# Optimization experiments

Hardware: AMD Instinct MI355X
Metric: run time of the kernel (lower is better)

The kernel has to match this reference:

```python
import jax, jax.numpy as jnp
import numpy as np

HIDDEN = 2048
NUM_HEADS = 16
HEAD_DIM = 128
WINDOW_SIZE = 512
NUM_GLOBAL = 16
SCALING = HEAD_DIM ** -0.5


def setup_inputs() -> dict:
    key = jax.random.key(0)
    ks = jax.random.split(key, 5)
    std = HIDDEN ** -0.5
    hidden_states = jax.random.normal(ks[0], (1, 4096, HIDDEN), dtype=jnp.float32)
    # Linear weights stored as (in, out) so y = x @ W
    Wq = jax.random.normal(ks[1], (HIDDEN, NUM_HEADS * HEAD_DIM), dtype=jnp.float32) * std
    Wk = jax.random.normal(ks[2], (HIDDEN, NUM_HEADS * HEAD_DIM), dtype=jnp.float32) * std
    Wv = jax.random.normal(ks[3], (HIDDEN, NUM_HEADS * HEAD_DIM), dtype=jnp.float32) * std
    Wo = jax.random.normal(ks[4], (NUM_HEADS * HEAD_DIM, HIDDEN), dtype=jnp.float32) * std
    return {"hidden_states": hidden_states, "Wq": Wq, "Wk": Wk, "Wv": Wv, "Wo": Wo}


def _sliding_mask(q_len: int, kv_len: int) -> jnp.ndarray:
    q_pos = jnp.arange(q_len)[:, None]
    kv_pos = jnp.arange(kv_len)[None, :]
    half_window = WINDOW_SIZE // 2
    local = jnp.abs(q_pos - kv_pos) < half_window
    glob = (q_pos < NUM_GLOBAL) | (kv_pos < NUM_GLOBAL)
    mask = local | glob
    return jnp.where(mask, 0.0, -jnp.inf).astype(jnp.float32)


def reference(hidden_states, Wq, Wk, Wv, Wo):
    bsz, q_len, _ = hidden_states.shape
    q = (hidden_states @ Wq).reshape(bsz, q_len, NUM_HEADS, HEAD_DIM).transpose(0, 2, 1, 3)
    k = (hidden_states @ Wk).reshape(bsz, q_len, NUM_HEADS, HEAD_DIM).transpose(0, 2, 1, 3)
    v = (hidden_states @ Wv).reshape(bsz, q_len, NUM_HEADS, HEAD_DIM).transpose(0, 2, 1, 3)
    mask = _sliding_mask(q_len, q_len)[None, None]  # [1,1,S,S]
    scores = jnp.einsum("bhqd,bhkd->bhqk", q, k) * SCALING + mask
    attn = jax.nn.softmax(scores.astype(jnp.float32), axis=-1).astype(q.dtype)
    out = jnp.einsum("bhqk,bhkd->bhqd", attn, v)
    out = out.transpose(0, 2, 1, 3).reshape(bsz, q_len, NUM_HEADS * HEAD_DIM)
    return out @ Wo
```

## Files before the change

kernel.cpp:

```cpp
#include <hip/hip_runtime.h>
#include <stdint.h>

#define SEQ    4096
#define HID    2048
#define NQKV   6144
#define QKW    4096
#define NH     16
#define HD     128
#define SCALE  0.08838834764831845f
#define GQC    32

typedef unsigned short u16;
typedef __attribute__((ext_vector_type(8))) short bf16x8;
typedef __attribute__((ext_vector_type(4))) float f32x4;

__device__ __forceinline__ u16 f2bf(float f) {
  union { float f; unsigned u; } v; v.f = f;
  unsigned r = v.u + 0x7FFFu + ((v.u >> 16) & 1u);
  return (u16)(r >> 16);
}

__device__ __forceinline__ float bf2f(u16 b) {
  union { unsigned u; float f; } c; c.u = ((unsigned)b) << 16; return c.f;
}

__device__ __forceinline__ void async16(const u16* g, u16* l) {
  __builtin_amdgcn_global_load_lds(
      (const __attribute__((address_space(1))) unsigned int*)g,
      (__attribute__((address_space(3))) unsigned int*)l, 16, 0, 0);
}

__global__ __launch_bounds__(256) void prep(const float* __restrict__ X,
                                            const float* __restrict__ W0,
                                            const float* __restrict__ W1,
                                            const float* __restrict__ W2,
                                            const float* __restrict__ W3,
                                            u16* __restrict__ Xbf,
                                            u16* __restrict__ Wcat,
                                            u16* __restrict__ Wot,
                                            unsigned* __restrict__ cnt) {
  const int bx = blockIdx.x;
  const int t = threadIdx.x;
  if (bx == 0 && t < NH) cnt[t] = 0u;
  if (bx < 8192) {
    int i = bx * 256 + t;
    float4 v = ((const float4*)X)[i];
    ushort4 o;
    o.x = f2bf(v.x); o.y = f2bf(v.y); o.z = f2bf(v.z); o.w = f2bf(v.w);
    ((ushort4*)Xbf)[i] = o;
    return;
  }
  __shared__ __align__(16) u16 Ts[64 * 68];
  const int b = bx - 8192;
  const int z = b >> 10;
  const int k0 = ((b >> 5) & 31) * 64;
  const int n0 = (b & 31) * 64;
  const float* W = (z == 0) ? W0 : (z == 1) ? W1 : (z == 2) ? W2 : W3;
  u16* Wt = (z < 3) ? (Wcat + (size_t)z * 2048 * 2048) : Wot;
#pragma unroll
  for (int p = 0; p < 4; ++p) {
    int f = (t + p * 256) * 4;
    int r = f >> 6, c = f & 63;
    float4 v = *(const float4*)&W[(size_t)(k0 + r) * 2048 + n0 + c];
    ushort4 o; o.x = f2bf(v.x); o.y = f2bf(v.y); o.z = f2bf(v.z); o.w = f2bf(v.w);
    *(ushort4*)&Ts[r * 68 + c] = o;
  }
  __syncthreads();
#pragma unroll
  for (int p = 0; p < 4; ++p) {
    int g = (t + p * 256) * 4;
    int r = g >> 6, c = g & 63;
    ushort4 o;
    o.x = Ts[(c + 0) * 68 + r];
    o.y = Ts[(c + 1) * 68 + r];
    o.z = Ts[(c + 2) * 68 + r];
    o.w = Ts[(c + 3) * 68 + r];
    *(ushort4*)&Wt[(size_t)(n0 + r) * 2048 + k0 + c] = o;
  }
}

template <typename OutT, bool WVT>
__global__ __launch_bounds__(256) void gemm_bt(const u16* __restrict__ A,
                                               const u16* __restrict__ B,
                                               OutT* __restrict__ C,
                                               u16* __restrict__ VTout,
                                               int K, int ldc) {
  __shared__ __align__(16) u16 As0[128 * 32];
  __shared__ __align__(16) u16 As1[128 * 32];
  __shared__ __align__(16) u16 Bs0[128 * 32];
  __shared__ __align__(16) u16 Bs1[128 * 32];
  const int m0 = blockIdx.y * 128;
  const int n0 = blockIdx.x * 128;
  const int tid = threadIdx.x;
  const int wid = tid >> 6;
  const int lane = tid & 63;
  const int wm = wid & 1, wn = wid >> 1;
  const int l15 = lane & 15, g4 = lane >> 4;

  const int srow = wid * 32 + (lane >> 2);
  const int scol = (lane & 3) * 8;

  f32x4 acc[4][4] = {};

  const u16* pa0 = &A[(size_t)(m0 + srow) * K + scol];
  const u16* pa1 = &A[(size_t)(m0 + srow + 16) * K + scol];
  const u16* pb0 = &B[(size_t)(n0 + srow) * K + scol];
  const u16* pb1 = &B[(size_t)(n0 + srow + 16) * K + scol];
  const int lo0 = (wid * 32) * 32, lo1 = (wid * 32 + 16) * 32;

  for (int kt = 0; kt < K; kt += 64) {
    __syncthreads();
    async16(pa0 + kt, &As0[lo0]);
    async16(pa1 + kt, &As0[lo1]);
    async16(pb0 + kt, &Bs0[lo0]);
    async16(pb1 + kt, &Bs0[lo1]);
    async16(pa0 + kt + 32, &As1[lo0]);
    async16(pa1 + kt + 32, &As1[lo1]);
    async16(pb0 + kt + 32, &Bs1[lo0]);
    async16(pb1 + kt + 32, &Bs1[lo1]);
    __syncthreads();
    {
      bf16x8 af[4], bfr[4];
#pragma unroll
      for (int i = 0; i < 4; ++i)
        af[i] = *(const bf16x8*)&As0[(wm * 64 + i * 16 + l15) * 32 + g4 * 8];
#pragma unroll
      for (int i = 0; i < 4; ++i)
        bfr[i] = *(const bf16x8*)&Bs0[(wn * 64 + i * 16 + l15) * 32 + g4 * 8];
#pragma unroll
      for (int mi = 0; mi < 4; ++mi)
#pragma unroll
        for (int ni = 0; ni < 4; ++ni)
          acc[mi][ni] = __builtin_amdgcn_mfma_f32_16x16x32_bf16(af[mi], bfr[ni], acc[mi][ni], 0, 0, 0);
    }
    {
      bf16x8 af[4], bfr[4];
#pragma unroll
      for (int i = 0; i < 4; ++i)
        af[i] = *(const bf16x8*)&As1[(wm * 64 + i * 16 + l15) * 32 + g4 * 8];
#pragma unroll
      for (int i = 0; i < 4; ++i)
        bfr[i] = *(const bf16x8*)&Bs1[(wn * 64 + i * 16 + l15) * 32 + g4 * 8];
#pragma unroll
      for (int mi = 0; mi < 4; ++mi)
#pragma unroll
        for (int ni = 0; ni < 4; ++ni)
          acc[mi][ni] = __builtin_amdgcn_mfma_f32_16x16x32_bf16(af[mi], bfr[ni], acc[mi][ni], 0, 0, 0);
    }
  }

  if (WVT && n0 >= QKW) {
#pragma unroll
    for (int mi = 0; mi < 4; ++mi)
#pragma unroll
      for (int ni = 0; ni < 4; ++ni) {
        const int nv = n0 - QKW + wn * 64 + ni * 16 + l15;
        const int hh = nv >> 7, dd = nv & 127;
        u16* base = &VTout[((size_t)hh * HD + dd) * SEQ];
        const int mb = m0 + wm * 64 + mi * 16 + g4 * 4;
        u16 pk[4];
#pragma unroll
        for (int r = 0; r < 4; ++r) pk[r] = f2bf(acc[mi][ni][r]);
        *(uint2*)&base[mb] = *(uint2*)pk;
      }
  } else {
#pragma unroll
    for (int mi = 0; mi < 4; ++mi)
#pragma unroll
      for (int ni = 0; ni < 4; ++ni) {
        const int n = n0 + wn * 64 + ni * 16 + l15;
#pragma unroll
        for (int r = 0; r < 4; ++r) {
          const int m = m0 + wm * 64 + mi * 16 + g4 * 4 + r;
          float v = acc[mi][ni][r];
          if constexpr (sizeof(OutT) == 2) {
            C[(size_t)m * ldc + n] = (OutT)f2bf(v);
          } else {
            C[(size_t)m * ldc + n] = v;
          }
        }
      }
  }
}

__device__ __forceinline__ void mfma16q(f32x4 (&q)[4][2],
                                        const bf16x8 (&a)[4][2],
                                        const bf16x8 (&b)[2][2]) {
#pragma unroll
  for (int fm = 0; fm < 4; ++fm)
#pragma unroll
    for (int fn = 0; fn < 2; ++fn) {
      q[fm][fn] = __builtin_amdgcn_mfma_f32_16x16x32_bf16(a[fm][0], b[fn][0], q[fm][fn], 0, 0, 0);
      q[fm][fn] = __builtin_amdgcn_mfma_f32_16x16x32_bf16(a[fm][1], b[fn][1], q[fm][fn], 0, 0, 0);
    }
}

#define GPRE() do { asm volatile("" ::: "memory"); __builtin_amdgcn_s_barrier(); \
  asm volatile("s_waitcnt lgkmcnt(0)" ::: "memory"); __builtin_amdgcn_sched_barrier(0); \
  __builtin_amdgcn_s_setprio(1); } while (0)
#define GPOST() do { __builtin_amdgcn_s_setprio(0); asm volatile("" ::: "memory"); \
  __builtin_amdgcn_s_barrier(); } while (0)
#define GPOSTVM() do { __builtin_amdgcn_s_setprio(0); \
  asm volatile("s_waitcnt vmcnt(4)" ::: "memory"); asm volatile("" ::: "memory"); \
  __builtin_amdgcn_s_barrier(); } while (0)

template <typename OutT, bool WVT>
__global__ __launch_bounds__(512, 2) void gemm256(const u16* __restrict__ A,
                                                  const u16* __restrict__ B,
                                                  OutT* __restrict__ C,
                                                  u16* __restrict__ VTout,
                                                  int K, int ldc) {
  __shared__ __align__(16) u16 As[2][2][128 * 64];
  __shared__ __align__(16) u16 Bs[2][2][128 * 64];
  const int m0 = blockIdx.y * 256;
  const int n0 = blockIdx.x * 256;
  const int tid = threadIdx.x;
  const int lane = tid & 63;
  const int wid = tid >> 6;
  const int wm = wid >> 2, wn = wid & 3;
  const int l15 = lane & 15, g4 = lane >> 4;

  const int r0 = tid >> 3;
  const int csw = ((tid & 7) ^ (r0 & 7)) * 8;
  const u16* Ag = A + (size_t)(m0 + r0) * K + csw;
  const u16* Bg = B + (size_t)(n0 + r0) * K + csw;

  const int aoff0 = (wm * 64 + l15) * 64;
  const int boff0 = (wn * 32 + l15) * 64;
  const int c0 = ((g4 ^ (l15 & 7)) << 3);
  const int c1 = (((4 + g4) ^ (l15 & 7)) << 3);

  auto stage = [&](const u16* src, int half, int tile, u16* dst) {
    const u16* s = src + (size_t)half * 128 * K + (size_t)tile * 64;
    u16* d = dst + wid * 512;
    async16(s, d);
    async16(s + (size_t)64 * K, d + 4096);
  };
  auto rdA = [&](const u16* h, bf16x8 (&a)[4][2]) {
#pragma unroll
    for (int fm = 0; fm < 4; ++fm) {
      a[fm][0] = *(const bf16x8*)&h[aoff0 + fm * 1024 + c0];
      a[fm][1] = *(const bf16x8*)&h[aoff0 + fm * 1024 + c1];
    }
  };
  auto rdB = [&](const u16* h, bf16x8 (&b)[2][2]) {
#pragma unroll
    for (int fn = 0; fn < 2; ++fn) {
      b[fn][0] = *(const bf16x8*)&h[boff0 + fn * 1024 + c0];
      b[fn][1] = *(const bf16x8*)&h[boff0 + fn * 1024 + c1];
    }
  };

  f32x4 acc[2][2][4][2] = {};

  stage(Ag, 0, 0, &As[0][0][0]);
  stage(Bg, 0, 0, &Bs[0][0][0]);
  stage(Ag, 1, 0, &As[0][1][0]);
  stage(Bg, 1, 0, &Bs[0][1][0]);
  stage(Ag, 0, 1, &As[1][0][0]);
  stage(Bg, 0, 1, &Bs[1][0][0]);
  asm volatile("s_waitcnt vmcnt(4)" ::: "memory");
  asm volatile("" ::: "memory");
  __builtin_amdgcn_s_barrier();

  const int NT = K >> 6;
  for (int it = 0; it < (NT >> 1); ++it) {
    const int tA = 2 * it + 1;
    const int tB = (2 * it + 2) & (NT - 1);
    const int tC = (2 * it + 3) & (NT - 1);
    {
      bf16x8 a0[4][2], a1[4][2], b0[2][2], b1[2][2];
      rdA(&As[0][0][0], a0); rdB(&Bs[0][0][0], b0);
      stage(Ag, 1, tA, &As[1][1][0]);
      asm volatile("s_waitcnt lgkmcnt(8)" ::: "memory");
      GPRE(); mfma16q(acc[0][0], a0, b0); GPOST();
      rdA(&As[0][1][0], a1);
      stage(Bg, 1, tA, &Bs[1][1][0]);
      GPRE(); mfma16q(acc[1][0], a1, b0); GPOST();
      rdB(&Bs[0][1][0], b1);
      stage(Ag, 0, tB, &As[0][0][0]);
      GPRE(); mfma16q(acc[0][1], a0, b1); GPOST();
      stage(Bg, 0, tB, &Bs[0][0][0]);
      GPRE(); mfma16q(acc[1][1], a1, b1); GPOSTVM();
    }
    {
      bf16x8 a0[4][2], a1[4][2], b0[2][2], b1[2][2];
      rdA(&As[1][0][0], a0); rdB(&Bs[1][0][0], b0);
      stage(Ag, 1, tB, &As[0][1][0]);
      asm volatile("s_waitcnt lgkmcnt(8)" ::: "memory");
      GPRE(); mfma16q(acc[0][0], a0, b0); GPOST();
      rdA(&As[1][1][0], a1);
      stage(Bg, 1, tB, &Bs[0][1][0]);
      GPRE(); mfma16q(acc[1][0], a1, b0); GPOST();
      rdB(&Bs[1][1][0], b1);
      stage(Ag, 0, tC, &As[1][0][0]);
      GPRE(); mfma16q(acc[0][1], a0, b1); GPOST();
      stage(Bg, 0, tC, &Bs[1][0][0]);
      GPRE(); mfma16q(acc[1][1], a1, b1); GPOSTVM();
    }
  }
  asm volatile("s_waitcnt vmcnt(0)" ::: "memory");

  if (WVT && n0 >= QKW) {
#pragma unroll
    for (int qm = 0; qm < 2; ++qm)
#pragma unroll
      for (int qn = 0; qn < 2; ++qn)
#pragma unroll
        for (int fm = 0; fm < 4; ++fm)
#pragma unroll
          for (int fn = 0; fn < 2; ++fn) {
            const int nv = n0 - QKW + qn * 128 + wn * 32 + fn * 16 + l15;
            const int hh = nv >> 7, dd = nv & 127;
            u16* base = &VTout[((size_t)hh * HD + dd) * SEQ];
            const int mb = m0 + qm * 128 + wm * 64 + fm * 16 + g4 * 4;
            u16 pk[4];
#pragma unroll
            for (int r = 0; r < 4; ++r) pk[r] = f2bf(acc[qm][qn][fm][fn][r]);
            *(uint2*)&base[mb] = *(uint2*)pk;
          }
  } else {
#pragma unroll
    for (int qm = 0; qm < 2; ++qm)
#pragma unroll
      for (int qn = 0; qn < 2; ++qn)
#pragma unroll
        for (int fm = 0; fm < 4; ++fm)
#pragma unroll
          for (int fn = 0; fn < 2; ++fn) {
            const int n = n0 + qn * 128 + wn * 32 + fn * 16 + l15;
#pragma unroll
            for (int r = 0; r < 4; ++r) {
              const int m = m0 + qm * 128 + wm * 64 + fm * 16 + g4 * 4 + r;
              float v = acc[qm][qn][fm][fn][r];
              if constexpr (sizeof(OutT) == 2) {
                C[(size_t)m * ldc + n] = (OutT)f2bf(v);
              } else {
                C[(size_t)m * ldc + n] = v;
              }
            }
          }
  }
}

__global__ __launch_bounds__(256, 2) void attn_fused(const u16* __restrict__ qk,
                                                     const u16* __restrict__ vt,
                                                     u16* __restrict__ out,
                                                     float* __restrict__ Opart,
                                                     float* __restrict__ MLpart,
                                                     unsigned* __restrict__ cnt) {
  __shared__ __align__(16) u16 smem[24576];
  __shared__ unsigned lastflag;
  const int h = blockIdx.y;
  const int tid = threadIdx.x;
  const int lane = tid & 63;

  if (blockIdx.x < 32) {
    u16* Ks  = smem;
    u16* VTs = smem + 8192;
    u16* Ps  = smem + 16384;
    const int q0 = blockIdx.x * 128;
    const int w = tid >> 6;
    const int l15 = lane & 15, g4 = lane >> 4, l7 = lane & 7;

    bf16x8 qf[2][4];
#pragma unroll
    for (int qs = 0; qs < 2; ++qs) {
      const u16* qrow = &qk[(size_t)(q0 + w * 32 + qs * 16 + l15) * QKW + h * HD + g4 * 8];
#pragma unroll
      for (int kk = 0; kk < 4; ++kk) qf[qs][kk] = *(const bf16x8*)&qrow[kk * 32];
    }

    float m_run[2] = {-1e30f, -1e30f}, l_run[2] = {0.f, 0.f};
    f32x4 o[2][8] = {};

    int lo = q0 - 255;
    int lo_blk = (lo < 0) ? 0 : (lo >> 6);
    int hi_blk = (q0 + 382) >> 6;
    if (hi_blk > 63) hi_blk = 63;
    const int extra = (lo_blk > 0) ? 1 : 0;
    const int nsteps = hi_blk - lo_blk + 1 + extra;

    for (int step = 0; step < nsteps; ++step) {
      const int kb = (extra && step == 0) ? 0 : (lo_blk + step - extra);
      const int kv0 = kb * 64;
      __syncthreads();
#pragma unroll
      for (int p = 0; p < 4; ++p) {
        const int r = w * 16 + p * 4 + (lane >> 4);
        const u16* src = &qk[(size_t)(kv0 + r) * QKW + 2048 + h * HD + (((lane & 15) ^ (r & 15)) * 8)];
        async16(src, &Ks[(w * 16 + p * 4) * 128]);
      }
#pragma unroll
      for (int p = 0; p < 4; ++p) {
        const int r = w * 32 + p * 8 + (lane >> 3);
        const u16* src = &vt[(size_t)h * (HD * SEQ) + (size_t)r * SEQ + kv0 + (((lane & 7) ^ (r & 7)) * 8)];
        async16(src, &VTs[(w * 32 + p * 8) * 64]);
      }
      __syncthreads();

      f32x4 st[2][4] = {};
#pragma unroll
      for (int kk = 0; kk < 4; ++kk) {
        bf16x8 ak[4];
#pragma unroll
        for (int t4 = 0; t4 < 4; ++t4)
          ak[t4] = *(const bf16x8*)&Ks[(t4 * 16 + l15) * 128 + (((kk * 4 + g4) ^ l15) * 8)];
#pragma unroll
        for (int qs = 0; qs < 2; ++qs)
#pragma unroll
          for (int t4 = 0; t4 < 4; ++t4)
            st[qs][t4] = __builtin_amdgcn_mfma_f32_16x16x32_bf16(ak[t4], qf[qs][kk], st[qs][t4], 0, 0, 0);
      }

#pragma unroll
      for (int qs = 0; qs < 2; ++qs) {
        const int q = q0 + w * 32 + qs * 16 + l15;
        float cmax = -1e30f;
#pragma unroll
        for (int t4 = 0; t4 < 4; ++t4)
#pragma unroll
          for (int r = 0; r < 4; ++r) {
            int kv = kv0 + t4 * 16 + g4 * 4 + r;
            int dq = q - kv; if (dq < 0) dq = -dq;
            bool ok = (dq < 256) || (kv < 16);
            float s = ok ? st[qs][t4][r] * SCALE : -1e30f;
            st[qs][t4][r] = s;
            cmax = fmaxf(cmax, s);
          }
        cmax = fmaxf(cmax, __shfl_xor(cmax, 16, 64));
        cmax = fmaxf(cmax, __shfl_xor(cmax, 32, 64));
        float mnew = fmaxf(m_run[qs], cmax);
        float csum = 0.f;
#pragma unroll
        for (int t4 = 0; t4 < 4; ++t4)
#pragma unroll
          for (int r = 0; r < 4; ++r) {
            float p = __expf(st[qs][t4][r] - mnew);
            st[qs][t4][r] = p;
            csum += p;
          }
        csum += __shfl_xor(csum, 16, 64);
        csum += __shfl_xor(csum, 32, 64);
        float a = __expf(m_run[qs] - mnew);
        m_run[qs] = mnew;
        l_run[qs] = l_run[qs] * a + csum;

#pragma unroll
        for (int t4 = 0; t4 < 4; ++t4) {
          u16 pk[4];
#pragma unroll
          for (int r = 0; r < 4; ++r) pk[r] = f2bf(st[qs][t4][r]);
          int c8 = t4 * 2 + (g4 >> 1);
          *(uint2*)&Ps[(w * 32 + qs * 16 + l15) * 64 + ((c8 ^ l7) * 8) + (g4 & 1) * 4] = *(uint2*)pk;
        }
#pragma unroll
        for (int nt = 0; nt < 8; ++nt)
#pragma unroll
          for (int r = 0; r < 4; ++r) o[qs][nt][r] *= a;
      }

#pragma unroll
      for (int ks = 0; ks < 2; ++ks) {
        bf16x8 ap[2];
#pragma unroll
        for (int qs = 0; qs < 2; ++qs)
          ap[qs] = *(const bf16x8*)&Ps[(w * 32 + qs * 16 + l15) * 64 + (((ks * 4 + g4) ^ l7) * 8)];
#pragma unroll
        for (int nt = 0; nt < 8; ++nt) {
          bf16x8 bv = *(const bf16x8*)&VTs[(nt * 16 + l15) * 64 + (((ks * 4 + g4) ^ l7) * 8)];
#pragma unroll
          for (int qs = 0; qs < 2; ++qs)
            o[qs][nt] = __builtin_amdgcn_mfma_f32_16x16x32_bf16(bv, ap[qs], o[qs][nt], 0, 0, 0);
        }
      }
    }

#pragma unroll
    for (int qs = 0; qs < 2; ++qs) {
      if (q0 + w * 32 + qs * 16 < 16) continue;
      const int q = q0 + w * 32 + qs * 16 + l15;
      const float inv = 1.f / l_run[qs];
#pragma unroll
      for (int nt = 0; nt < 8; ++nt) {
        u16 pk[4];
#pragma unroll
        for (int r = 0; r < 4; ++r) pk[r] = f2bf(o[qs][nt][r] * inv);
        *(uint2*)&out[(size_t)q * HID + h * HD + nt * 16 + g4 * 4] = *(uint2*)pk;
      }
    }
    return;
  }

  {
    u16* Ks = smem;
    u16* Vs = smem + 8704;
    const int chunk = blockIdx.x - 32;
    const int t = tid;
    const int q = t >> 4, dg = t & 15;

    float qr[8];
    {
      bf16x8 v = *(const bf16x8*)&qk[(size_t)q * QKW + h * HD + dg * 8];
#pragma unroll
      for (int j = 0; j < 8; ++j) qr[j] = bf2f((u16)v[j]);
    }
    float m_run = -1e30f, l_run = 0.f, o[8] = {};
    const int kvbase = chunk * (SEQ / GQC);

    for (int st = 0; st < (SEQ / GQC) / 64; ++st) {
      const int kv0 = kvbase + st * 64;
      __syncthreads();
#pragma unroll
      for (int p = 0; p < 4; ++p) {
        int f = (t + p * 256) * 8;
        int r = f >> 7, c = f & 127;
        *(uint4*)&Ks[r * 136 + c] = *(const uint4*)&qk[(size_t)(kv0 + r) * QKW + 2048 + h * HD + c];
      }
#pragma unroll
      for (int p = 0; p < 4; ++p) {
        int id = p * 256 + t;
        int d = id >> 3, c8 = id & 7;
        uint4 v = *(const uint4*)&vt[(size_t)h * (HD * SEQ) + (size_t)d * SEQ + kv0 + c8 * 8];
        const u16* pv16 = (const u16*)&v;
#pragma unroll
        for (int j = 0; j < 8; ++j) Vs[(c8 * 8 + j) * 136 + d] = pv16[j];
      }
      __syncthreads();
      for (int kv = 0; kv < 64; ++kv) {
        bf16x8 kr = *(const bf16x8*)&Ks[kv * 136 + dg * 8];
        float s = 0.f;
#pragma unroll
        for (int j = 0; j < 8; ++j) s += qr[j] * bf2f((u16)kr[j]);
        s += __shfl_xor(s, 1, 64); s += __shfl_xor(s, 2, 64);
        s += __shfl_xor(s, 4, 64); s += __shfl_xor(s, 8, 64);
        s *= SCALE;
        float mnew = fmaxf(m_run, s);
        float alpha = __expf(m_run - mnew);
        float p = __expf(s - mnew);
        m_run = mnew;
        l_run = l_run * alpha + p;
        bf16x8 vr = *(const bf16x8*)&Vs[kv * 136 + dg * 8];
#pragma unroll
        for (int j = 0; j < 8; ++j) o[j] = o[j] * alpha + p * bf2f((u16)vr[j]);
      }
    }
    float* op = &Opart[(((size_t)h * GQC + chunk) * 16 + q) * HD + dg * 8];
#pragma unroll
    for (int j = 0; j < 8; ++j) op[j] = o[j];
    if (dg == 0) {
      float* ml = &MLpart[(((size_t)h * GQC + chunk) * 16 + q) * 2];
      ml[0] = m_run; ml[1] = l_run;
    }

    __syncthreads();
    if (t == 0) {
      __threadfence();
      lastflag = (atomicAdd(&cnt[h], 1u) == GQC - 1) ? 1u : 0u;
    }
    __syncthreads();
    if (lastflag) {
      __threadfence();
      float M = -1e30f;
      for (int c = 0; c < GQC; ++c)
        M = fmaxf(M, MLpart[(((size_t)h * GQC + c) * 16 + q) * 2]);
      float L = 0.f, oo[8] = {};
      for (int c = 0; c < GQC; ++c) {
        const float* ml = &MLpart[(((size_t)h * GQC + c) * 16 + q) * 2];
        float e = __expf(ml[0] - M);
        L += e * ml[1];
        const float* opc = &Opart[(((size_t)h * GQC + c) * 16 + q) * HD + dg * 8];
#pragma unroll
        for (int j = 0; j < 8; ++j) oo[j] += e * opc[j];
      }
      float inv = 1.f / L;
      u16 tmp[8];
#pragma unroll
      for (int j = 0; j < 8; ++j) tmp[j] = f2bf(oo[j] * inv);
      *(uint4*)&out[(size_t)q * HID + h * HD + dg * 8] = *(uint4*)tmp;
    }
  }
}

extern "C" void kernel_launch(void* const* d_in, const int* in_sizes, int n_in,
                              void* d_out, int out_size, void* d_ws, size_t ws_size,
                              hipStream_t stream) {
  const float* X  = (const float*)d_in[0];
  const float* Wq = (const float*)d_in[1];
  const float* Wk = (const float*)d_in[2];
  const float* Wv = (const float*)d_in[3];
  const float* Wo = (const float*)d_in[4];
  float* out = (float*)d_out;

  char* ws = (char*)d_ws;
  u16* Xbf    = (u16*)(ws);
  u16* Wcat   = (u16*)(ws + (size_t)(16 << 20));
  u16* AttnO  = (u16*)(ws + (size_t)(16 << 20));
  float* Opart  = (float*)(ws + (size_t)(32 << 20));
  float* MLpart = (float*)(ws + (size_t)(36 << 20));
  unsigned* cnt = (unsigned*)d_out;
  u16* QK     = (u16*)(ws + (size_t)(40 << 20));
  u16* VT     = (u16*)(ws + (size_t)(72 << 20));
  u16* Wot    = (u16*)(ws + (size_t)(88 << 20));

  prep<<<dim3(12288), 256, 0, stream>>>(X, Wq, Wk, Wv, Wo, Xbf, Wcat, Wot, cnt);
  gemm256<u16, true><<<dim3(24, 16), 512, 0, stream>>>(Xbf, Wcat, QK, VT, HID, QKW);
  attn_fused<<<dim3(32 + GQC, NH), 256, 0, stream>>>(QK, VT, AttnO, Opart, MLpart, cnt);
  gemm_bt<float, false><<<dim3(16, 32), 256, 0, stream>>>(AttnO, Wot, out, nullptr, HID, HID);
}
```

Before: 412.6 us.

## Software-pipeline LDS fragment reads one phase ahead in GEMM main loop

Restructures the 256x256 GEMM main loop into eight uniform phases that each prefetch the next phase's LDS fragments into persistent registers while the current quadrant's MFMAs run. Quadrant order is changed to a snake pattern (00,01,11,10) so each phase reloads only one of the A or B fragments. The lgkmcnt waits are partial and the vmcnt depth rises to allow more outstanding global loads. This aims to hide LDS read latency behind MFMA work and cut barrier stalls, at the cost of more live registers and tighter correctness reliance on hand-tuned waitcnt counts.

```diff
diff --git a/kernel.cpp b/kernel.cpp
--- a/kernel.cpp
+++ b/kernel.cpp
@@ -195,14 +195,21 @@
     }
 }
 
-#define GPRE() do { asm volatile("" ::: "memory"); __builtin_amdgcn_s_barrier(); \
-  asm volatile("s_waitcnt lgkmcnt(0)" ::: "memory"); __builtin_amdgcn_sched_barrier(0); \
-  __builtin_amdgcn_s_setprio(1); } while (0)
-#define GPOST() do { __builtin_amdgcn_s_setprio(0); asm volatile("" ::: "memory"); \
-  __builtin_amdgcn_s_barrier(); } while (0)
-#define GPOSTVM() do { __builtin_amdgcn_s_setprio(0); \
-  asm volatile("s_waitcnt vmcnt(4)" ::: "memory"); asm volatile("" ::: "memory"); \
-  __builtin_amdgcn_s_barrier(); } while (0)
+#define PH(RD_STMT, SRC, HALF, TILE, SLOT, NLG, ACCQ, ASET, BSET)      \
+  do {                                                                  \
+    RD_STMT;                                                            \
+    stage(SRC, HALF, TILE, SLOT);                                       \
+    asm volatile("" ::: "memory");                                      \
+    __builtin_amdgcn_s_barrier();                                       \
+    asm volatile("s_waitcnt lgkmcnt(" #NLG ")" ::: "memory");           \
+    __builtin_amdgcn_sched_barrier(0);                                  \
+    __builtin_amdgcn_s_setprio(1);                                      \
+    mfma16q(ACCQ, ASET, BSET);                                          \
+    __builtin_amdgcn_s_setprio(0);                                      \
+    asm volatile("s_waitcnt vmcnt(6)" ::: "memory");                    \
+    asm volatile("" ::: "memory");                                      \
+    __builtin_amdgcn_s_barrier();                                       \
+  } while (0)
 
 template <typename OutT, bool WVT>
 __global__ __launch_bounds__(512, 2) void gemm256(const u16* __restrict__ A,
@@ -252,54 +259,35 @@
   };
 
   f32x4 acc[2][2][4][2] = {};
+  bf16x8 aX[4][2], aY[4][2], bU[2][2], bV[2][2];
 
   stage(Ag, 0, 0, &As[0][0][0]);
   stage(Bg, 0, 0, &Bs[0][0][0]);
+  stage(Bg, 1, 0, &Bs[0][1][0]);
   stage(Ag, 1, 0, &As[0][1][0]);
-  stage(Bg, 1, 0, &Bs[0][1][0]);
   stage(Ag, 0, 1, &As[1][0][0]);
   stage(Bg, 0, 1, &Bs[1][0][0]);
-  asm volatile("s_waitcnt vmcnt(4)" ::: "memory");
+  asm volatile("s_waitcnt vmcnt(6)" ::: "memory");
   asm volatile("" ::: "memory");
   __builtin_amdgcn_s_barrier();
+  rdA(&As[0][0][0], aX);
+  rdB(&Bs[0][0][0], bU);
 
   const int NT = K >> 6;
   for (int it = 0; it < (NT >> 1); ++it) {
     const int tA = 2 * it + 1;
     const int tB = (2 * it + 2) & (NT - 1);
     const int tC = (2 * it + 3) & (NT - 1);
-    {
-      bf16x8 a0[4][2], a1[4][2], b0[2][2], b1[2][2];
-      rdA(&As[0][0][0], a0); rdB(&Bs[0][0][0], b0);
-      stage(Ag, 1, tA, &As[1][1][0]);
-      asm volatile("s_waitcnt lgkmcnt(8)" ::: "memory");
-      GPRE(); mfma16q(acc[0][0], a0, b0); GPOST();
-      rdA(&As[0][1][0], a1);
-      stage(Bg, 1, tA, &Bs[1][1][0]);
-      GPRE(); mfma16q(acc[1][0], a1, b0); GPOST();
-      rdB(&Bs[0][1][0], b1);
-      stage(Ag, 0, tB, &As[0][0][0]);
-      GPRE(); mfma16q(acc[0][1], a0, b1); GPOST();
-      stage(Bg, 0, tB, &Bs[0][0][0]);
-      GPRE(); mfma16q(acc[1][1], a1, b1); GPOSTVM();
-    }
-    {
-      bf16x8 a0[4][2], a1[4][2], b0[2][2], b1[2][2];
-      rdA(&As[1][0][0], a0); rdB(&Bs[1][0][0], b0);
-      stage(Ag, 1, tB, &As[0][1][0]);
-      asm volatile("s_waitcnt lgkmcnt(8)" ::: "memory");
-      GPRE(); mfma16q(acc[0][0], a0, b0); GPOST();
-      rdA(&As[1][1][0], a1);
-      stage(Bg, 1, tB, &Bs[0][1][0]);
-      GPRE(); mfma16q(acc[1][0], a1, b0); GPOST();
-      rdB(&Bs[1][1][0], b1);
-      stage(Ag, 0, tC, &As[1][0][0]);
-      GPRE(); mfma16q(acc[0][1], a0, b1); GPOST();
-      stage(Bg, 0, tC, &Bs[1][0][0]);
-      GPRE(); mfma16q(acc[1][1], a1, b1); GPOSTVM();
-    }
-  }
-  asm volatile("s_waitcnt vmcnt(0)" ::: "memory");
+    PH(rdB(&Bs[0][1][0], bV), Bg, 1, tA, &Bs[1][1][0], 4,  acc[0][0], aX, bU);
+    PH(rdA(&As[0][1][0], aY), Ag, 1, tA, &As[1][1][0], 8,  acc[0][1], aX, bV);
+    PH(rdA(&As[1][0][0], aX), Ag, 0, tB, &As[0][0][0], 8,  acc[1][1], aY, bV);
+    PH(rdB(&Bs[1][0][0], bV), Bg, 0, tB, &Bs[0][0][0], 12, acc[1][0], aY, bU);
+    PH(rdB(&Bs[1][1][0], bU), Bg, 1, tB, &Bs[0][1][0], 4,  acc[0][0], aX, bV);
+    PH(rdA(&As[1][1][0], aY), Ag, 1, tB, &As[0][1][0], 8,  acc[0][1], aX, bU);
+    PH(rdA(&As[0][0][0], aX), Ag, 0, tC, &As[1][0][0], 8,  acc[1][1], aY, bU);
+    PH(rdB(&Bs[0][0][0], bU), Bg, 0, tC, &Bs[1][0][0], 12, acc[1][0], aY, bV);
+  }
+  asm volatile("s_waitcnt vmcnt(0) lgkmcnt(0)" ::: "memory");
 
   if (WVT && n0 >= QKW) {
 #pragma unroll
```

Measured after the change: 420.0 us. Within noise of the previous version (+1.8%).
